# Performance work log

Measured on AMD Instinct MI355X. Metric: run time of the kernel, lower is better.

Reference implementation:

```python
import jax, jax.numpy as jnp
import numpy as np


def log_g(x):
    # log of g(x) = x+0.5 if x>=0 else sigmoid(x), computed stably
    return jnp.where(x >= 0, jnp.log(jax.nn.relu(x) + 0.5), -jax.nn.softplus(-x))


def setup_inputs() -> dict:
    key = jax.random.key(0)
    ks = jax.random.split(key, 6)
    B, S, D, H = 8, 4096, 1024, 1024
    scale = 1.0 / np.sqrt(D)
    return {
        "x": jax.random.normal(ks[0], (B, S, D), dtype=jnp.float32),
        "h0": jax.random.normal(ks[1], (B, 1, H), dtype=jnp.float32),
        "Wz": jax.random.normal(ks[2], (H, D), dtype=jnp.float32) * scale,
        "bz": jax.random.normal(ks[3], (H,), dtype=jnp.float32) * scale,
        "Wh": jax.random.normal(ks[4], (H, D), dtype=jnp.float32) * scale,
        "bh": jax.random.normal(ks[5], (H,), dtype=jnp.float32) * scale,
    }


def reference(x, h0, Wz, bz, Wh, bh):
    # x: (B,S,D), h0: (B,1,H)
    k = jnp.einsum("bsd,hd->bsh", x, Wz) + bz            # linear_z
    log_z = -jax.nn.softplus(-k)                          # log sigmoid(k)
    log_coeffs = -jax.nn.softplus(k)                      # log (1 - sigmoid(k))
    log_h0 = log_g(h0)                                    # (B,1,H)
    log_tilde_h = log_g(jnp.einsum("bsd,hd->bsh", x, Wh) + bh)
    log_values = jnp.concatenate([log_h0, log_z + log_tilde_h], axis=1)  # (B,S+1,H)
    a_star = jnp.pad(jnp.cumsum(log_coeffs, axis=1), ((0, 0), (1, 0), (0, 0)))  # (B,S+1,H)
    log_h0_plus_b_star = jax.lax.cumlogsumexp(log_values - a_star, axis=1)
    h = jnp.exp(a_star[:, 1:] + log_h0_plus_b_star[:, 1:])  # (B,S,H)
    return h
```

## Files before the change

### kernel.cpp

```cpp
#include <hip/hip_runtime.h>
#include <cstdint>
#include <cstddef>

#define B_  8
#define S_  4096
#define D_  1024
#define H_  1024
#define M_  (B_*S_)
#define NT_ 2048
#define NC_ 64
#define L_  (S_/NC_)

typedef __bf16 bf16x8 __attribute__((ext_vector_type(8)));
typedef float  f32x4  __attribute__((ext_vector_type(4)));
typedef uint16_t u16x8 __attribute__((ext_vector_type(8)));

__device__ __forceinline__ uint16_t f2bf(float f) {
  union { float f; uint32_t u; } v; v.f = f;
  uint32_t u = v.u;
  u += 0x7FFFu + ((u >> 16) & 1u);
  return (uint16_t)(u >> 16);
}
__device__ __forceinline__ float gfun(float x) {
  return x >= 0.0f ? x + 0.5f
                   : __builtin_amdgcn_rcpf(1.0f + __expf(-x));
}
__device__ __forceinline__ void unpack_cv(uint32_t u, float& c, float& v) {
  union { uint32_t u; _Float16 h[2]; } p; p.u = u;
  c = (float)p.h[0]; v = (float)p.h[1];
}

#define X8_  (M_ * D_ / 8)
#define W8_  (H_ * D_ / 8)
#define TOT8_ (X8_ + 2 * W8_)
__global__ __launch_bounds__(256) void cvt_all_kernel(
    const float* __restrict__ x, const float* __restrict__ Wz,
    const float* __restrict__ Wh, uint16_t* __restrict__ xb,
    uint16_t* __restrict__ Wc) {
  int stride = gridDim.x * 256;
  for (int u = blockIdx.x * 256 + threadIdx.x; u < TOT8_; u += stride) {
    const float* src; uint16_t* dst;
    if (u < X8_) {
      src = x + (size_t)u * 8; dst = xb + (size_t)u * 8;
    } else if (u < X8_ + W8_) {
      int v = u - X8_;
      int r = v >> 7, c = v & 127;
      int row = ((r >> 4) << 5) | (r & 15);
      src = Wz + (size_t)v * 8;
      dst = Wc + (size_t)row * D_ + c * 8;
    } else {
      int v = u - X8_ - W8_;
      int r = v >> 7, c = v & 127;
      int row = ((r >> 4) << 5) | 16 | (r & 15);
      src = Wh + (size_t)v * 8;
      dst = Wc + (size_t)row * D_ + c * 8;
    }
    float4 a = ((const float4*)src)[0], b = ((const float4*)src)[1];
    u16x8 o;
    o[0] = f2bf(a.x); o[1] = f2bf(a.y); o[2] = f2bf(a.z); o[3] = f2bf(a.w);
    o[4] = f2bf(b.x); o[5] = f2bf(b.y); o[6] = f2bf(b.z); o[7] = f2bf(b.w);
    *(u16x8*)dst = o;
  }
}

#define BK 64
__global__ __launch_bounds__(512, 2)
void fused_gemm_kernel(const uint16_t* __restrict__ A,
                       const uint16_t* __restrict__ Wc,
                       const float* __restrict__ bz,
                       const float* __restrict__ bh,
                       uint32_t* __restrict__ cv) {
  __shared__ __attribute__((aligned(16))) uint16_t sA[2][256 * BK];
  __shared__ __attribute__((aligned(16))) uint16_t sB[2][256 * BK];

  const int tid  = threadIdx.x;
  const int lane = tid & 63;
  const int wave = tid >> 6;
  const int wm = wave >> 2;
  const int wn = wave & 3;
  const int q  = lane >> 4;
  const int mn = lane & 15;

  const int bid  = blockIdx.x;
  const int tile = (bid & 7) * 128 + (bid >> 3);
  const int mTile = (tile >> 3) * 256;
  const int nTile = (tile & 7) * 256;

  const int rl = tid >> 3;
  const int cu = tid & 7;
  const int sw = cu ^ (rl & 7);
  const uint16_t* aSrc[4];
  const uint16_t* bSrc[4];
  #pragma unroll
  for (int L = 0; L < 4; L++) {
    aSrc[L] = A  + (size_t)(mTile + L * 64 + rl) * D_ + sw * 8;
    bSrc[L] = Wc + (size_t)(nTile + L * 64 + rl) * D_ + sw * 8;
  }
  const int ldsSlot = tid * 8;

  const int swr = mn & 7;
  const int aBase = (wm * 128 + mn) * 64;
  const int bBase = (wn * 64  + mn) * 64;
  int koff[2];
  #pragma unroll
  for (int kk = 0; kk < 2; kk++) koff[kk] = ((kk * 4 + q) ^ swr) * 8;

#define STAGE_A(buf, kt, L)                                                    \
  __builtin_amdgcn_global_load_lds(                                            \
      (const __attribute__((address_space(1))) void*)(aSrc[L] + (kt) * BK),    \
      (__attribute__((address_space(3))) void*)&sA[buf][(L) * 4096 + ldsSlot], \
      16, 0, 0)
#define STAGE_B(buf, kt, L)                                                    \
  __builtin_amdgcn_global_load_lds(                                            \
      (const __attribute__((address_space(1))) void*)(bSrc[L] + (kt) * BK),    \
      (__attribute__((address_space(3))) void*)&sB[buf][(L) * 4096 + ldsSlot], \
      16, 0, 0)

  f32x4 acc[8][4] = {};

  STAGE_A(0, 0, 0); STAGE_A(0, 0, 2);
  STAGE_B(0, 0, 0); STAGE_B(0, 0, 1); STAGE_B(0, 0, 2); STAGE_B(0, 0, 3);
  STAGE_A(0, 0, 1); STAGE_A(0, 0, 3);
  STAGE_A(1, 1, 0); STAGE_A(1, 1, 2);
  STAGE_B(1, 1, 0); STAGE_B(1, 1, 1); STAGE_B(1, 1, 2); STAGE_B(1, 1, 3);
  STAGE_A(1, 1, 1); STAGE_A(1, 1, 3);
  asm volatile("s_waitcnt vmcnt(8)" ::: "memory");
  __builtin_amdgcn_s_barrier();
  __builtin_amdgcn_sched_barrier(0);

  #pragma unroll 2
  for (int t = 0; t < D_ / BK - 1; ++t) {
    const int curb = t & 1, nxtb = curb ^ 1;
    const uint16_t* sAc = sA[curb];
    const uint16_t* sBc = sB[curb];
    const bool doStage = (t >= 1);
    const int kn = t + 1;

    bf16x8 bv[4][2];

    #pragma unroll
    for (int p = 0; p < 4; ++p) {
      if (p == 0) {
        #pragma unroll
        for (int tn = 0; tn < 4; tn++)
          #pragma unroll
          for (int kk = 0; kk < 2; kk++)
            bv[tn][kk] = *(const bf16x8*)&sBc[bBase + tn * 1024 + koff[kk]];
      }
      bf16x8 av[2][2];
      #pragma unroll
      for (int mi = 0; mi < 2; mi++)
        #pragma unroll
        for (int kk = 0; kk < 2; kk++)
          av[mi][kk] =
              *(const bf16x8*)&sAc[aBase + (2 * p + mi) * 1024 + koff[kk]];

      if (doStage) {
        if (p == 0) { STAGE_A(nxtb, kn, 0); STAGE_A(nxtb, kn, 2); }
        if (p == 1) { STAGE_B(nxtb, kn, 0); STAGE_B(nxtb, kn, 1); }
        if (p == 2) { STAGE_B(nxtb, kn, 2); STAGE_B(nxtb, kn, 3); }
        if (p == 3) { STAGE_A(nxtb, kn, 1); STAGE_A(nxtb, kn, 3); }
      }

      __builtin_amdgcn_s_setprio(1);
      #pragma unroll
      for (int mi = 0; mi < 2; mi++)
        #pragma unroll
        for (int tn = 0; tn < 4; tn++)
          #pragma unroll
          for (int kk = 0; kk < 2; kk++)
            acc[2 * p + mi][tn] = __builtin_amdgcn_mfma_f32_16x16x32_bf16(
                av[mi][kk], bv[tn][kk], acc[2 * p + mi][tn], 0, 0, 0);
      __builtin_amdgcn_s_setprio(0);

      if (p == 1) asm volatile("s_waitcnt vmcnt(4)" ::: "memory");
      if (p == 3) asm volatile("s_waitcnt vmcnt(2)" ::: "memory");
      __builtin_amdgcn_s_barrier();
      __builtin_amdgcn_sched_barrier(0);
    }
  }
#undef STAGE_A
#undef STAGE_B

  asm volatile("s_waitcnt vmcnt(0)" ::: "memory");
  __builtin_amdgcn_s_barrier();
  __builtin_amdgcn_sched_barrier(0);
  {
    const uint16_t* sAc = sA[1];
    const uint16_t* sBc = sB[1];
    bf16x8 bv[4][2];
    #pragma unroll
    for (int tn = 0; tn < 4; tn++)
      #pragma unroll
      for (int kk = 0; kk < 2; kk++)
        bv[tn][kk] = *(const bf16x8*)&sBc[bBase + tn * 1024 + koff[kk]];
    __builtin_amdgcn_s_setprio(1);
    #pragma unroll
    for (int m = 0; m < 8; m++) {
      bf16x8 av[2];
      #pragma unroll
      for (int kk = 0; kk < 2; kk++)
        av[kk] = *(const bf16x8*)&sAc[aBase + m * 1024 + koff[kk]];
      #pragma unroll
      for (int tn = 0; tn < 4; tn++)
        #pragma unroll
        for (int kk = 0; kk < 2; kk++)
          acc[m][tn] = __builtin_amdgcn_mfma_f32_16x16x32_bf16(
              av[kk], bv[tn][kk], acc[m][tn], 0, 0, 0);
    }
    __builtin_amdgcn_s_setprio(0);
  }

  #pragma unroll
  for (int tp = 0; tp < 2; ++tp) {
    const int ncol = nTile + wn * 64 + tp * 32;
    const int h = ((ncol >> 5) << 4) + mn;
    const float bzc = bz[h], bhc = bh[h];
    #pragma unroll
    for (int m = 0; m < 8; ++m) {
      const int row0 = mTile + wm * 128 + m * 16 + q * 4;
      #pragma unroll
      for (int i = 0; i < 4; ++i) {
        float kv = acc[m][2 * tp][i] + bzc;
        float pv = acc[m][2 * tp + 1][i] + bhc;
        float c = __builtin_amdgcn_rcpf(1.0f + __expf(kv));
        float v = (1.0f - c) * gfun(pv);
        union { _Float16 h2[2]; uint32_t u; } pk;
        pk.h2[0] = (_Float16)c; pk.h2[1] = (_Float16)v;
        cv[(size_t)(row0 + i) * H_ + h] = pk.u;
      }
    }
  }
}

__global__ __launch_bounds__(256) void scan_chunk_kernel(
    const uint32_t* __restrict__ cv, float4* __restrict__ Cc,
    float4* __restrict__ Vc) {
  const int tid = threadIdx.x;
  const int nc = blockIdx.x, b = blockIdx.y;
  const uint4* cv4 = (const uint4*)cv;
  size_t base = (size_t)(b * S_ + nc * L_) * (H_ / 4) + tid;
  float C[4] = {1.f, 1.f, 1.f, 1.f};
  float V[4] = {0.f, 0.f, 0.f, 0.f};
  #pragma unroll 4
  for (int t = 0; t < L_; t++) {
    uint4 w = cv4[base + (size_t)t * (H_ / 4)];
    float c, v;
    unpack_cv(w.x, c, v); C[0] *= c; V[0] = c * V[0] + v;
    unpack_cv(w.y, c, v); C[1] *= c; V[1] = c * V[1] + v;
    unpack_cv(w.z, c, v); C[2] *= c; V[2] = c * V[2] + v;
    unpack_cv(w.w, c, v); C[3] *= c; V[3] = c * V[3] + v;
  }
  size_t o = (size_t)(b * NC_ + nc) * (H_ / 4) + tid;
  Cc[o] = (float4){C[0], C[1], C[2], C[3]};
  Vc[o] = (float4){V[0], V[1], V[2], V[3]};
}

__global__ __launch_bounds__(256) void scan_apply_kernel(
    const uint32_t* __restrict__ cv, const float4* __restrict__ Cc,
    const float4* __restrict__ Vc, const float* __restrict__ h0,
    float4* __restrict__ out) {
  const int tid = threadIdx.x;
  const int nc = blockIdx.x, b = blockIdx.y;
  const uint4* cv4 = (const uint4*)cv;

  float Hr[4];
  #pragma unroll
  for (int j = 0; j < 4; j++) Hr[j] = gfun(h0[(size_t)b * H_ + tid * 4 + j]);
  #pragma unroll 4
  for (int j = 0; j < nc; j++) {
    size_t idx = (size_t)(b * NC_ + j) * (H_ / 4) + tid;
    float4 Cq = Cc[idx], Vq = Vc[idx];
    Hr[0] = Cq.x * Hr[0] + Vq.x;
    Hr[1] = Cq.y * Hr[1] + Vq.y;
    Hr[2] = Cq.z * Hr[2] + Vq.z;
    Hr[3] = Cq.w * Hr[3] + Vq.w;
  }

  size_t base = (size_t)(b * S_ + nc * L_) * (H_ / 4) + tid;
  #pragma unroll 4
  for (int t = 0; t < L_; t++) {
    size_t idx = base + (size_t)t * (H_ / 4);
    uint4 w = cv4[idx];
    float c, v;
    unpack_cv(w.x, c, v); Hr[0] = c * Hr[0] + v;
    unpack_cv(w.y, c, v); Hr[1] = c * Hr[1] + v;
    unpack_cv(w.z, c, v); Hr[2] = c * Hr[2] + v;
    unpack_cv(w.w, c, v); Hr[3] = c * Hr[3] + v;
    out[idx] = (float4){Hr[0], Hr[1], Hr[2], Hr[3]};
  }
}

extern "C" void kernel_launch(void* const* d_in, const int* in_sizes, int n_in,
                              void* d_out, int out_size, void* d_ws, size_t ws_size,
                              hipStream_t stream) {
  const float* x  = (const float*)d_in[0];
  const float* h0 = (const float*)d_in[1];
  const float* Wz = (const float*)d_in[2];
  const float* bz = (const float*)d_in[3];
  const float* Wh = (const float*)d_in[4];
  const float* bh = (const float*)d_in[5];
  float* out = (float*)d_out;

  char* ws = (char*)d_ws;
  uint16_t* xb  = (uint16_t*)ws; ws += (size_t)M_ * D_ * 2;
  uint16_t* Wcb = (uint16_t*)ws; ws += (size_t)NT_ * D_ * 2;
  uint32_t* cvb = (uint32_t*)ws; ws += (size_t)M_ * H_ * 4;
  char* alias = (char*)xb;
  float* Cc  = (float*)alias; alias += (size_t)B_ * NC_ * H_ * 4;
  float* Vc  = (float*)alias; alias += (size_t)B_ * NC_ * H_ * 4;

  cvt_all_kernel<<<dim3(2048), 256, 0, stream>>>(x, Wz, Wh, xb, Wcb);

  fused_gemm_kernel<<<dim3((NT_ / 256) * (M_ / 256)), 512, 0, stream>>>(
      xb, Wcb, bz, bh, cvb);

  scan_chunk_kernel<<<dim3(NC_, B_), 256, 0, stream>>>(cvb, (float4*)Cc, (float4*)Vc);
  scan_apply_kernel<<<dim3(NC_, B_), 256, 0, stream>>>(
      cvb, (const float4*)Cc, (const float4*)Vc, h0, (float4*)out);
}
```

Before: 446.8 us.

## Fuse chunk-level scan reduction into GEMM epilogue and add prefix kernel

```diff
diff --git a/kernel.cpp b/kernel.cpp
--- a/kernel.cpp
+++ b/kernel.cpp
@@ -69,7 +69,9 @@
                        const uint16_t* __restrict__ Wc,
                        const float* __restrict__ bz,
                        const float* __restrict__ bh,
-                       uint32_t* __restrict__ cv) {
+                       uint32_t* __restrict__ cv,
+                       float* __restrict__ Sc,
+                       float* __restrict__ Sv) {
   __shared__ __attribute__((aligned(16))) uint16_t sA[2][256 * BK];
   __shared__ __attribute__((aligned(16))) uint16_t sB[2][256 * BK];
 
@@ -211,14 +213,18 @@
     __builtin_amdgcn_s_setprio(0);
   }
 
+  const int bIdx = mTile >> 12;
+  const int nc0  = (mTile & (S_ - 1)) >> 6;
   #pragma unroll
   for (int tp = 0; tp < 2; ++tp) {
     const int ncol = nTile + wn * 64 + tp * 32;
     const int h = ((ncol >> 5) << 4) + mn;
     const float bzc = bz[h], bhc = bh[h];
+    float Cr = 1.0f, Vr = 0.0f;
     #pragma unroll
     for (int m = 0; m < 8; ++m) {
       const int row0 = mTile + wm * 128 + m * 16 + q * 4;
+      float Ct = 1.0f, Vt = 0.0f;
       #pragma unroll
       for (int i = 0; i < 4; ++i) {
         float kv = acc[m][2 * tp][i] + bzc;
@@ -228,37 +234,52 @@
         union { _Float16 h2[2]; uint32_t u; } pk;
         pk.h2[0] = (_Float16)c; pk.h2[1] = (_Float16)v;
         cv[(size_t)(row0 + i) * H_ + h] = pk.u;
+        float cr_ = (float)pk.h2[0], vr_ = (float)pk.h2[1];
+        Vt = cr_ * Vt + vr_;
+        Ct = Ct * cr_;
+      }
+      {
+        float Cp = __shfl_xor(Ct, 16), Vp = __shfl_xor(Vt, 16);
+        Vt = (q & 1) ? (Ct * Vp + Vt) : (Cp * Vt + Vp);
+        Ct = Ct * Cp;
+        Cp = __shfl_xor(Ct, 32); Vp = __shfl_xor(Vt, 32);
+        Vt = (q & 2) ? (Ct * Vp + Vt) : (Cp * Vt + Vp);
+        Ct = Ct * Cp;
+      }
+      if ((m & 3) == 0) { Cr = Ct; Vr = Vt; }
+      else             { Vr = Ct * Vr + Vt; Cr = Cr * Ct; }
+      if ((m & 3) == 3) {
+        if (q == 0) {
+          const int nc = nc0 + wm * 2 + (m >> 2);
+          const size_t sidx = ((size_t)(bIdx * NC_ + nc) << 10) + h;
+          Sc[sidx] = Cr;
+          Sv[sidx] = Vr;
+        }
+        Cr = 1.0f; Vr = 0.0f;
       }
     }
   }
 }
 
-__global__ __launch_bounds__(256) void scan_chunk_kernel(
-    const uint32_t* __restrict__ cv, float4* __restrict__ Cc,
-    float4* __restrict__ Vc) {
-  const int tid = threadIdx.x;
-  const int nc = blockIdx.x, b = blockIdx.y;
-  const uint4* cv4 = (const uint4*)cv;
-  size_t base = (size_t)(b * S_ + nc * L_) * (H_ / 4) + tid;
-  float C[4] = {1.f, 1.f, 1.f, 1.f};
-  float V[4] = {0.f, 0.f, 0.f, 0.f};
+__global__ __launch_bounds__(256) void prefix_kernel(
+    const float* __restrict__ Sc, const float* __restrict__ Sv,
+    float* __restrict__ Pc, float* __restrict__ Pv) {
+  const int u = blockIdx.x * 256 + threadIdx.x;
+  const int b = u >> 10, h = u & 1023;
+  float C = 1.0f, V = 0.0f;
   #pragma unroll 4
-  for (int t = 0; t < L_; t++) {
-    uint4 w = cv4[base + (size_t)t * (H_ / 4)];
-    float c, v;
-    unpack_cv(w.x, c, v); C[0] *= c; V[0] = c * V[0] + v;
-    unpack_cv(w.y, c, v); C[1] *= c; V[1] = c * V[1] + v;
-    unpack_cv(w.z, c, v); C[2] *= c; V[2] = c * V[2] + v;
-    unpack_cv(w.w, c, v); C[3] *= c; V[3] = c * V[3] + v;
-  }
-  size_t o = (size_t)(b * NC_ + nc) * (H_ / 4) + tid;
-  Cc[o] = (float4){C[0], C[1], C[2], C[3]};
-  Vc[o] = (float4){V[0], V[1], V[2], V[3]};
+  for (int nc = 0; nc < NC_; nc++) {
+    const size_t idx = ((size_t)(b * NC_ + nc) << 10) + h;
+    Pc[idx] = C; Pv[idx] = V;
+    const float sc = Sc[idx], sv = Sv[idx];
+    V = sc * V + sv;
+    C = C * sc;
+  }
 }
 
 __global__ __launch_bounds__(256) void scan_apply_kernel(
-    const uint32_t* __restrict__ cv, const float4* __restrict__ Cc,
-    const float4* __restrict__ Vc, const float* __restrict__ h0,
+    const uint32_t* __restrict__ cv, const float4* __restrict__ Pc,
+    const float4* __restrict__ Pv, const float* __restrict__ h0,
     float4* __restrict__ out) {
   const int tid = threadIdx.x;
   const int nc = blockIdx.x, b = blockIdx.y;
@@ -267,10 +288,9 @@
   float Hr[4];
   #pragma unroll
   for (int j = 0; j < 4; j++) Hr[j] = gfun(h0[(size_t)b * H_ + tid * 4 + j]);
-  #pragma unroll 4
-  for (int j = 0; j < nc; j++) {
-    size_t idx = (size_t)(b * NC_ + j) * (H_ / 4) + tid;
-    float4 Cq = Cc[idx], Vq = Vc[idx];
+  {
+    const size_t pidx = (size_t)(b * NC_ + nc) * (H_ / 4) + tid;
+    const float4 Cq = Pc[pidx], Vq = Pv[pidx];
     Hr[0] = Cq.x * Hr[0] + Vq.x;
     Hr[1] = Cq.y * Hr[1] + Vq.y;
     Hr[2] = Cq.z * Hr[2] + Vq.z;
@@ -307,15 +327,18 @@
   uint16_t* Wcb = (uint16_t*)ws; ws += (size_t)NT_ * D_ * 2;
   uint32_t* cvb = (uint32_t*)ws; ws += (size_t)M_ * H_ * 4;
   char* alias = (char*)xb;
-  float* Cc  = (float*)alias; alias += (size_t)B_ * NC_ * H_ * 4;
-  float* Vc  = (float*)alias; alias += (size_t)B_ * NC_ * H_ * 4;
+  float* Pc = (float*)alias; alias += (size_t)B_ * NC_ * H_ * 4;
+  float* Pv = (float*)alias; alias += (size_t)B_ * NC_ * H_ * 4;
+  float* Sc = out;
+  float* Sv = out + (size_t)B_ * NC_ * H_;
 
   cvt_all_kernel<<<dim3(2048), 256, 0, stream>>>(x, Wz, Wh, xb, Wcb);
 
   fused_gemm_kernel<<<dim3((NT_ / 256) * (M_ / 256)), 512, 0, stream>>>(
-      xb, Wcb, bz, bh, cvb);
-
-  scan_chunk_kernel<<<dim3(NC_, B_), 256, 0, stream>>>(cvb, (float4*)Cc, (float4*)Vc);
+      xb, Wcb, bz, bh, cvb, Sc, Sv);
+
+  prefix_kernel<<<dim3(B_ * H_ / 256), 256, 0, stream>>>(Sc, Sv, Pc, Pv);
+
   scan_apply_kernel<<<dim3(NC_, B_), 256, 0, stream>>>(
-      cvb, (const float4*)Cc, (const float4*)Vc, h0, (float4*)out);
-}
+      cvb, (const float4*)Pc, (const float4*)Pv, h0, (float4*)out);
+}
```

New measurement: 442.2 us. About the same (-1.0%).
